# Kernel optimization log

Hardware: AMD Instinct MI355X
Metric: run time of the kernel (lower is better)

## Reference

```python
import jax, jax.numpy as jnp
import numpy as np

N = 100000      # nodes
E = 1600000     # edges (avg degree 16)
IN_DIM = 64
H = 4           # num_heads
D = 32          # out_dim per head
NEG_SLOPE = 0.1


def setup_inputs() -> dict:
    key = jax.random.key(0)
    k_x, k_src, k_dst, k_w, k_fc, k_al, k_ar = jax.random.split(key, 7)
    x = jax.random.normal(k_x, (N, IN_DIM), dtype=jnp.float32)
    src = jax.random.randint(k_src, (E,), 0, N, dtype=jnp.int32)
    dst = jax.random.randint(k_dst, (E,), 0, N, dtype=jnp.int32)
    w = jax.random.uniform(k_w, (E,), dtype=jnp.float32)
    # xavier-ish init for learned params
    W_fc = jax.random.normal(k_fc, (IN_DIM, H * D), dtype=jnp.float32) * (2.0 / (IN_DIM + H * D)) ** 0.5
    attn_l = jax.random.normal(k_al, (1, H, D), dtype=jnp.float32) * 0.1
    attn_r = jax.random.normal(k_ar, (1, H, D), dtype=jnp.float32) * 0.1
    vt = jnp.zeros((1,), dtype=jnp.float32)  # unused by forward (as in the source)
    return {"vt": vt, "x": x, "src": src, "dst": dst, "w": w,
            "W_fc": W_fc, "attn_l": attn_l, "attn_r": attn_r}


def reference(vt, x, src, dst, w, W_fc, attn_l, attn_r):
    # node projection: [N, H, D]
    feat = (x @ W_fc).reshape(-1, H, D)
    el = jnp.sum(feat * attn_l, axis=-1)  # [N, H]
    er = jnp.sum(feat * attn_r, axis=-1)  # [N, H]
    # per-edge logits: u_add_v then leaky_relu, scaled by edge weight w
    e = el[src] + er[dst]                                   # [E, H]
    e = jnp.where(e >= 0, e, NEG_SLOPE * e)                 # leaky_relu
    e = w[:, None] * e                                      # [E, H]
    # edge softmax grouped by destination node (numerically stable)
    m = jax.ops.segment_max(e, dst, num_segments=N)         # [N, H]
    ex = jnp.exp(e - m[dst])                                # [E, H]
    den = jax.ops.segment_sum(ex, dst, num_segments=N)      # [N, H]
    a = ex / den[dst]                                       # [E, H]
    # message passing: u_mul_e -> sum over incoming edges
    msg = feat[src] * a[:, :, None]                         # [E, H, D]
    out = jax.ops.segment_sum(msg, dst, num_segments=N)     # [N, H, D]
    return out
```

## Files before the change

### kernel.cpp

```cpp
#include <hip/hip_runtime.h>
#include <math.h>

#define IN_DIM 64
#define HH 4
#define CC 128
#define NEG_SLOPE 0.1f

typedef __attribute__((ext_vector_type(8))) short short8;
typedef __attribute__((ext_vector_type(4))) float f32x4;

__device__ __forceinline__ float leaky(float v) { return v >= 0.f ? v : NEG_SLOPE * v; }

__device__ __forceinline__ unsigned f2bf(float f) {
  unsigned u = __float_as_uint(f);
  unsigned r = u + 0x7FFFu + ((u >> 16) & 1u);
  return r >> 16;
}
__device__ __forceinline__ float bflo(unsigned v) { return __uint_as_float(v << 16); }
__device__ __forceinline__ float bfhi(unsigned v) { return __uint_as_float(v & 0xFFFF0000u); }

__global__ void k_prepw(const float* __restrict__ W, unsigned* __restrict__ wt) {
  int tid = blockIdx.x * 256 + threadIdx.x;
  if (tid >= 128 * 32) return;
  int n = tid >> 5;
  int r = tid & 31;
  int b = r >> 2, h = r & 3;
  int k = b * 8 + h * 2;
  unsigned lo = f2bf(W[k * CC + n]);
  unsigned hi = f2bf(W[(k + 1) * CC + n]);
  wt[n * 32 + (b ^ (n & 7)) * 4 + h] = lo | (hi << 16);
}

__global__ __launch_bounds__(256) void k_project(
    const float* __restrict__ x, const unsigned* __restrict__ wt,
    const float* __restrict__ attn_l, const float* __restrict__ attn_r,
    unsigned* __restrict__ featbf, float* __restrict__ el, float* __restrict__ er,
    int N)
{
  __shared__ unsigned Wlds[4096];
  __shared__ float Al[CC], Ar[CC];
  int t = threadIdx.x;
  {
    const uint4* s = (const uint4*)wt;
    uint4* d = (uint4*)Wlds;
#pragma unroll
    for (int i = 0; i < 4; ++i) d[t + 256 * i] = s[t + 256 * i];
  }
  if (t < CC) { Al[t] = attn_l[t]; Ar[t] = attn_r[t]; }
  __syncthreads();

  int lane = t & 63;
  int l4 = lane >> 4, l16 = lane & 15;
  int node = blockIdx.x * 64 + (t >> 6) * 16 + l16;
  bool valid = node < N;
  int nrow = valid ? node : 0;

  short8 bfr[2];
#pragma unroll
  for (int s = 0; s < 2; ++s) {
    const float4* xp = (const float4*)&x[(size_t)nrow * 64 + s * 32 + l4 * 8];
    float4 xa = xp[0], xb = xp[1];
    union { short8 v; unsigned u[4]; } pk;
    pk.u[0] = f2bf(xa.x) | (f2bf(xa.y) << 16);
    pk.u[1] = f2bf(xa.z) | (f2bf(xa.w) << 16);
    pk.u[2] = f2bf(xb.x) | (f2bf(xb.y) << 16);
    pk.u[3] = f2bf(xb.z) | (f2bf(xb.w) << 16);
    bfr[s] = pk.v;
  }

  f32x4 acc[8];
#pragma unroll
  for (int c = 0; c < 8; ++c) acc[c] = (f32x4){0.f, 0.f, 0.f, 0.f};

#pragma unroll
  for (int c = 0; c < 8; ++c) {
    int n0 = c * 16 + l16;
    int sw = n0 & 7;
#pragma unroll
    for (int s = 0; s < 2; ++s) {
      int b = s * 4 + l4;
      union { short8 v; uint4 q; } af;
      af.q = *(const uint4*)&Wlds[n0 * 32 + (b ^ sw) * 4];
      acc[c] = __builtin_amdgcn_mfma_f32_16x16x32_bf16(af.v, bfr[s], acc[c], 0, 0, 0);
    }
  }

  if (valid) {
#pragma unroll
    for (int c = 0; c < 8; ++c) {
      unsigned u0 = f2bf(acc[c][0]) | (f2bf(acc[c][1]) << 16);
      unsigned u1 = f2bf(acc[c][2]) | (f2bf(acc[c][3]) << 16);
      *(uint2*)&featbf[(size_t)node * 64 + c * 8 + l4 * 2] = make_uint2(u0, u1);
    }
  }

  float pl[4], pr[4];
#pragma unroll
  for (int h = 0; h < 4; ++h) {
    float sl = 0.f, sr = 0.f;
#pragma unroll
    for (int ct = 0; ct < 2; ++ct) {
      int c = 2 * h + ct;
      int cb = c * 16 + l4 * 4;
#pragma unroll
      for (int r = 0; r < 4; ++r) {
        sl = fmaf(acc[c][r], Al[cb + r], sl);
        sr = fmaf(acc[c][r], Ar[cb + r], sr);
      }
    }
    sl += __shfl_xor(sl, 16, 64); sl += __shfl_xor(sl, 32, 64);
    sr += __shfl_xor(sr, 16, 64); sr += __shfl_xor(sr, 32, 64);
    pl[h] = sl; pr[h] = sr;
  }
  if (l4 == 0 && valid) {
    *(float4*)&el[(size_t)node * 4] = make_float4(pl[0], pl[1], pl[2], pl[3]);
    *(float4*)&er[(size_t)node * 4] = make_float4(pr[0], pr[1], pr[2], pr[3]);
  }
}

__global__ __launch_bounds__(256) void k_bhist(const int* __restrict__ dst,
                                               int* __restrict__ bcnt, int E, int NB) {
  __shared__ int lh[512];
  for (int i = threadIdx.x; i < NB; i += 256) lh[i] = 0;
  __syncthreads();
  int stride = gridDim.x * 256;
  for (int i = blockIdx.x * 256 + threadIdx.x; i < E; i += stride)
    atomicAdd(&lh[dst[i] >> 8], 1);
  __syncthreads();
  for (int i = threadIdx.x; i < NB; i += 256) {
    int c = lh[i];
    if (c) atomicAdd(&bcnt[i], c);
  }
}

__global__ __launch_bounds__(512) void k_bscan(const int* __restrict__ bcnt,
                                               int* __restrict__ gbase,
                                               int* __restrict__ gcursor, int NB) {
  __shared__ int sh[512];
  int t = threadIdx.x;
  int v = (t < NB) ? bcnt[t] : 0;
  sh[t] = v;
  __syncthreads();
  for (int off = 1; off < 512; off <<= 1) {
    int a = (t >= off) ? sh[t - off] : 0;
    __syncthreads();
    sh[t] += a;
    __syncthreads();
  }
  if (t < NB) {
    int e = sh[t] - v;
    gbase[t] = e;
    gcursor[t] = e;
  }
}

__global__ __launch_bounds__(512) void k_binA(const int* __restrict__ src,
                                              const int* __restrict__ dst,
                                              const float* __restrict__ w,
                                              int* __restrict__ gcursor,
                                              uint2* __restrict__ bkt, int E, int NB) {
  __shared__ int lh[512];
  __shared__ int lbase[512];
  int t = threadIdx.x;
  for (int i = t; i < NB; i += 512) lh[i] = 0;
  __syncthreads();
  long eb = (long)blockIdx.x * 8192;
  int b[16]; int r[16]; unsigned px[16]; unsigned pw[16];
#pragma unroll
  for (int i = 0; i < 16; ++i) {
    long e = eb + t + i * 512;
    bool v = e < E;
    int d = v ? dst[e] : 0;
    b[i] = d >> 8;
    px[i] = v ? ((unsigned)src[e] | ((unsigned)(d & 255) << 20)) : 0u;
    pw[i] = v ? ((const unsigned*)w)[e] : 0u;
    r[i] = v ? atomicAdd(&lh[b[i]], 1) : -1;
  }
  __syncthreads();
  for (int i = t; i < NB; i += 512) {
    int c = lh[i];
    lbase[i] = c ? atomicAdd(&gcursor[i], c) : 0;
  }
  __syncthreads();
#pragma unroll
  for (int i = 0; i < 16; ++i)
    if (r[i] >= 0) bkt[lbase[b[i]] + r[i]] = make_uint2(px[i], pw[i]);
}

__global__ __launch_bounds__(256) void k_binB(const uint2* __restrict__ bkt,
                                              const int* __restrict__ bcnt,
                                              const int* __restrict__ gbase,
                                              int* __restrict__ offs,
                                              int2* __restrict__ sp,
                                              int N, int E, int NB) {
  __shared__ int lh[256], sc[256], lcur[256];
  int b = blockIdx.x;
  int t = threadIdx.x;
  int base_b = gbase[b];
  int cnt_b = bcnt[b];
  lh[t] = 0;
  __syncthreads();
  for (int e = t; e < cnt_b; e += 256) {
    uint2 p = bkt[base_b + e];
    atomicAdd(&lh[(p.x >> 20) & 255], 1);
  }
  __syncthreads();
  int v = lh[t];
  sc[t] = v;
  __syncthreads();
  for (int off = 1; off < 256; off <<= 1) {
    int a = (t >= off) ? sc[t - off] : 0;
    __syncthreads();
    sc[t] += a;
    __syncthreads();
  }
  int excl = sc[t] - v;
  lcur[t] = excl;
  int n0 = b << 8;
  if (n0 + t < N) offs[n0 + t] = base_b + excl;
  if (b == NB - 1 && t == 0) offs[N] = E;
  __syncthreads();
  for (int e = t; e < cnt_b; e += 256) {
    uint2 p = bkt[base_b + e];
    int d = (p.x >> 20) & 255;
    int pos = atomicAdd(&lcur[d], 1);
    sp[base_b + pos] = make_int2((int)(p.x & 0xFFFFFu), (int)p.y);
  }
}

__global__ __launch_bounds__(256) void k_aggregate(
    const int* __restrict__ offs, const int2* __restrict__ sp,
    const float* __restrict__ el, const float* __restrict__ er,
    const uint2* __restrict__ featbf, float* __restrict__ out, int N)
{
  __shared__ int   s_lds[4][64];
  __shared__ float4 a_lds[4][64];

  int t = threadIdx.x;
  int lane = t & 63, wv = t >> 6;
  int n = blockIdx.x * 4 + wv;
  if (n >= N) return;

  int off0 = offs[n], off1 = offs[n + 1];
  int deg = off1 - off0;
  int half = lane >> 5;
  int l32 = lane & 31;
  int h = l32 >> 3;
  float4 acc = make_float4(0.f, 0.f, 0.f, 0.f);

  if (deg > 0) {
    float4 erv = *reinterpret_cast<const float4*>(&er[n * HH]);
    if (deg <= 64) {
      bool act = lane < deg;
      int2 p = sp[off0 + (act ? lane : 0)];
      int s = p.x;
      float wgt = __int_as_float(p.y);
      float4 elv = *reinterpret_cast<const float4*>(&el[s * HH]);
      float e0 = act ? leaky(elv.x + erv.x) * wgt : -INFINITY;
      float e1 = act ? leaky(elv.y + erv.y) * wgt : -INFINITY;
      float e2 = act ? leaky(elv.z + erv.z) * wgt : -INFINITY;
      float e3 = act ? leaky(elv.w + erv.w) * wgt : -INFINITY;
      float m0 = e0, m1 = e1, m2 = e2, m3 = e3;
#pragma unroll
      for (int d = 32; d >= 1; d >>= 1) {
        m0 = fmaxf(m0, __shfl_xor(m0, d, 64));
        m1 = fmaxf(m1, __shfl_xor(m1, d, 64));
        m2 = fmaxf(m2, __shfl_xor(m2, d, 64));
        m3 = fmaxf(m3, __shfl_xor(m3, d, 64));
      }
      float x0 = act ? __expf(e0 - m0) : 0.f;
      float x1 = act ? __expf(e1 - m1) : 0.f;
      float x2 = act ? __expf(e2 - m2) : 0.f;
      float x3 = act ? __expf(e3 - m3) : 0.f;
      float d0 = x0, d1 = x1, d2 = x2, d3 = x3;
#pragma unroll
      for (int d = 32; d >= 1; d >>= 1) {
        d0 += __shfl_xor(d0, d, 64);
        d1 += __shfl_xor(d1, d, 64);
        d2 += __shfl_xor(d2, d, 64);
        d3 += __shfl_xor(d3, d, 64);
      }
      float a0 = x0 * __builtin_amdgcn_rcpf(d0);
      float a1 = x1 * __builtin_amdgcn_rcpf(d1);
      float a2 = x2 * __builtin_amdgcn_rcpf(d2);
      float a3 = x3 * __builtin_amdgcn_rcpf(d3);
      s_lds[wv][lane] = s;
      a_lds[wv][lane] = make_float4(a0, a1, a2, a3);

      int npair = (deg + 1) >> 1;
      for (int tt = 0; tt < npair; ++tt) {
        int idx = 2 * tt + half;
        bool vv = idx < deg;
        float a = vv ? reinterpret_cast<const float*>(&a_lds[wv][idx])[h] : 0.f;
        int sj = s_lds[wv][vv ? idx : 0];
        uint2 f = featbf[(size_t)sj * 32 + l32];
        acc.x = fmaf(a, bflo(f.x), acc.x);
        acc.y = fmaf(a, bfhi(f.x), acc.y);
        acc.z = fmaf(a, bflo(f.y), acc.z);
        acc.w = fmaf(a, bfhi(f.y), acc.w);
      }
    } else {
      float m0 = -INFINITY, m1 = -INFINITY, m2 = -INFINITY, m3 = -INFINITY;
      for (int base = off0; base < off1; base += 64) {
        int j = base + lane;
        bool act = j < off1;
        int2 p = sp[act ? j : off0];
        float wgt = __int_as_float(p.y);
        float4 elv = *reinterpret_cast<const float4*>(&el[p.x * HH]);
        float e0 = act ? leaky(elv.x + erv.x) * wgt : -INFINITY;
        float e1 = act ? leaky(elv.y + erv.y) * wgt : -INFINITY;
        float e2 = act ? leaky(elv.z + erv.z) * wgt : -INFINITY;
        float e3 = act ? leaky(elv.w + erv.w) * wgt : -INFINITY;
        m0 = fmaxf(m0, e0); m1 = fmaxf(m1, e1);
        m2 = fmaxf(m2, e2); m3 = fmaxf(m3, e3);
      }
#pragma unroll
      for (int d = 32; d >= 1; d >>= 1) {
        m0 = fmaxf(m0, __shfl_xor(m0, d, 64));
        m1 = fmaxf(m1, __shfl_xor(m1, d, 64));
        m2 = fmaxf(m2, __shfl_xor(m2, d, 64));
        m3 = fmaxf(m3, __shfl_xor(m3, d, 64));
      }
      float d0 = 0.f, d1 = 0.f, d2 = 0.f, d3 = 0.f;
      for (int base = off0; base < off1; base += 64) {
        int j = base + lane;
        bool act = j < off1;
        int2 p = sp[act ? j : off0];
        float wgt = __int_as_float(p.y);
        float4 elv = *reinterpret_cast<const float4*>(&el[p.x * HH]);
        float e0 = leaky(elv.x + erv.x) * wgt;
        float e1 = leaky(elv.y + erv.y) * wgt;
        float e2 = leaky(elv.z + erv.z) * wgt;
        float e3 = leaky(elv.w + erv.w) * wgt;
        d0 += act ? __expf(e0 - m0) : 0.f;
        d1 += act ? __expf(e1 - m1) : 0.f;
        d2 += act ? __expf(e2 - m2) : 0.f;
        d3 += act ? __expf(e3 - m3) : 0.f;
      }
#pragma unroll
      for (int d = 32; d >= 1; d >>= 1) {
        d0 += __shfl_xor(d0, d, 64);
        d1 += __shfl_xor(d1, d, 64);
        d2 += __shfl_xor(d2, d, 64);
        d3 += __shfl_xor(d3, d, 64);
      }
      float i0 = __builtin_amdgcn_rcpf(d0), i1 = __builtin_amdgcn_rcpf(d1);
      float i2 = __builtin_amdgcn_rcpf(d2), i3 = __builtin_amdgcn_rcpf(d3);
      for (int base = off0; base < off1; base += 64) {
        int j = base + lane;
        bool act = j < off1;
        int2 p = sp[act ? j : off0];
        float wgt = __int_as_float(p.y);
        float4 elv = *reinterpret_cast<const float4*>(&el[p.x * HH]);
        float e0 = leaky(elv.x + erv.x) * wgt;
        float e1 = leaky(elv.y + erv.y) * wgt;
        float e2 = leaky(elv.z + erv.z) * wgt;
        float e3 = leaky(elv.w + erv.w) * wgt;
        float a0 = act ? __expf(e0 - m0) * i0 : 0.f;
        float a1 = act ? __expf(e1 - m1) * i1 : 0.f;
        float a2 = act ? __expf(e2 - m2) * i2 : 0.f;
        float a3 = act ? __expf(e3 - m3) * i3 : 0.f;
        s_lds[wv][lane] = p.x;
        a_lds[wv][lane] = make_float4(a0, a1, a2, a3);
        int cnt = off1 - base; if (cnt > 64) cnt = 64;
        int npair = (cnt + 1) >> 1;
        for (int tt = 0; tt < npair; ++tt) {
          int idx = 2 * tt + half;
          bool vv = idx < cnt;
          float a = vv ? reinterpret_cast<const float*>(&a_lds[wv][idx])[h] : 0.f;
          int sj = s_lds[wv][vv ? idx : 0];
          uint2 f = featbf[(size_t)sj * 32 + l32];
          acc.x = fmaf(a, bflo(f.x), acc.x);
          acc.y = fmaf(a, bfhi(f.x), acc.y);
          acc.z = fmaf(a, bflo(f.y), acc.z);
          acc.w = fmaf(a, bfhi(f.y), acc.w);
        }
      }
    }
  }
  acc.x += __shfl_xor(acc.x, 32, 64);
  acc.y += __shfl_xor(acc.y, 32, 64);
  acc.z += __shfl_xor(acc.z, 32, 64);
  acc.w += __shfl_xor(acc.w, 32, 64);
  if (lane < 32)
    *reinterpret_cast<float4*>(&out[(size_t)n * CC + 4 * l32]) = acc;
}

extern "C" void kernel_launch(void* const* d_in, const int* in_sizes, int n_in,
                              void* d_out, int out_size, void* d_ws, size_t ws_size,
                              hipStream_t stream)
{
  const float* x      = (const float*)d_in[1];
  const int*   src    = (const int*)d_in[2];
  const int*   dst    = (const int*)d_in[3];
  const float* w      = (const float*)d_in[4];
  const float* W_fc   = (const float*)d_in[5];
  const float* attn_l = (const float*)d_in[6];
  const float* attn_r = (const float*)d_in[7];
  float* out = (float*)d_out;

  int N = in_sizes[1] / IN_DIM;
  int E = in_sizes[2];
  int NB = (N + 255) / 256;

  char* p = (char*)d_ws;
  auto alloc = [&](size_t bytes) {
    char* r = p;
    p += (bytes + 255) & ~size_t(255);
    return r;
  };
  unsigned* featbf = (unsigned*)alloc((size_t)N * 64 * 4);
  float* el    = (float*)alloc((size_t)N * HH * 4);
  float* er    = (float*)alloc((size_t)N * HH * 4);
  int*   offs  = (int*)alloc((size_t)(N + 1) * 4);
  int*   bcnt  = (int*)alloc(512 * 4);
  int*   gbase = (int*)alloc(512 * 4);
  int*   gcur  = (int*)alloc(512 * 4);
  unsigned* wtswz = (unsigned*)alloc(4096 * 4);
  uint2* bkt   = (uint2*)alloc((size_t)E * 8);
  int2*  sp    = (int2*)alloc((size_t)E * 8);

  hipMemsetAsync(bcnt, 0, 512 * 4, stream);

  k_prepw<<<16, 256, 0, stream>>>(W_fc, wtswz);
  k_project<<<(N + 63) / 64, 256, 0, stream>>>(x, wtswz, attn_l, attn_r, featbf, el, er, N);
  k_bhist<<<256, 256, 0, stream>>>(dst, bcnt, E, NB);
  k_bscan<<<1, 512, 0, stream>>>(bcnt, gbase, gcur, NB);
  k_binA<<<(E + 8191) / 8192, 512, 0, stream>>>(src, dst, w, gcur, bkt, E, NB);
  k_binB<<<NB, 256, 0, stream>>>(bkt, bcnt, gbase, offs, sp, N, E, NB);
  k_aggregate<<<(N + 3) / 4, 256, 0, stream>>>(offs, sp, el, er, (const uint2*)featbf, out, N);
}
```

Baseline: 152.5 us.

## Split aggregation into alpha pass and column-sliced gather with quantized attention

Replaces the fused softmax+gather kernel with two passes. The first computes per-edge softmax weights and packs them, quantized to 12 bits, with the 20-bit source index into per-head arrays. The second gathers from a feature array re-laid out as 8 column slices so each slice fits better in cache. The intent is better cache locality for the random feature gather and less per-edge metadata traffic. The cost is an extra pass over the edges and 12-bit attention quantization, which lowers accuracy, plus a 20-bit limit on node indices.

After: 264.7 us. 1.74x slower.

```diff
diff --git a/kernel.cpp b/kernel.cpp
--- a/kernel.cpp
+++ b/kernel.cpp
@@ -34,7 +34,7 @@
 __global__ __launch_bounds__(256) void k_project(
     const float* __restrict__ x, const unsigned* __restrict__ wt,
     const float* __restrict__ attn_l, const float* __restrict__ attn_r,
-    unsigned* __restrict__ featbf, float* __restrict__ el, float* __restrict__ er,
+    unsigned* __restrict__ featS, float* __restrict__ el, float* __restrict__ er,
     int N)
 {
   __shared__ unsigned Wlds[4096];
@@ -90,7 +90,7 @@
     for (int c = 0; c < 8; ++c) {
       unsigned u0 = f2bf(acc[c][0]) | (f2bf(acc[c][1]) << 16);
       unsigned u1 = f2bf(acc[c][2]) | (f2bf(acc[c][3]) << 16);
-      *(uint2*)&featbf[(size_t)node * 64 + c * 8 + l4 * 2] = make_uint2(u0, u1);
+      *(uint2*)&featS[((size_t)c * N + node) * 8 + l4 * 2] = make_uint2(u0, u1);
     }
   }
 
@@ -228,162 +228,172 @@
   }
 }
 
-__global__ __launch_bounds__(256) void k_aggregate(
+__global__ __launch_bounds__(256) void k_alpha(
     const int* __restrict__ offs, const int2* __restrict__ sp,
     const float* __restrict__ el, const float* __restrict__ er,
-    const uint2* __restrict__ featbf, float* __restrict__ out, int N)
+    unsigned* __restrict__ AQ0, unsigned* __restrict__ AQ1,
+    unsigned* __restrict__ AQ2, unsigned* __restrict__ AQ3, int N)
 {
-  __shared__ int   s_lds[4][64];
-  __shared__ float4 a_lds[4][64];
-
-  int t = threadIdx.x;
-  int lane = t & 63, wv = t >> 6;
-  int n = blockIdx.x * 4 + wv;
+  int t = threadIdx.x;
+  int lane = t & 63;
+  int half = lane >> 5, l32 = lane & 31;
+  int n = blockIdx.x * 8 + (t >> 6) * 2 + half;
   if (n >= N) return;
-
   int off0 = offs[n], off1 = offs[n + 1];
   int deg = off1 - off0;
-  int half = lane >> 5;
-  int l32 = lane & 31;
-  int h = l32 >> 3;
-  float4 acc = make_float4(0.f, 0.f, 0.f, 0.f);
-
-  if (deg > 0) {
-    float4 erv = *reinterpret_cast<const float4*>(&er[n * HH]);
-    if (deg <= 64) {
-      bool act = lane < deg;
-      int2 p = sp[off0 + (act ? lane : 0)];
-      int s = p.x;
+  if (deg <= 0) return;
+  float4 erv = *(const float4*)&er[(size_t)n * 4];
+
+  if (deg <= 32) {
+    bool act = l32 < deg;
+    int j = off0 + (act ? l32 : 0);
+    int2 p = sp[j];
+    float wgt = __int_as_float(p.y);
+    float4 elv = *(const float4*)&el[(size_t)p.x * 4];
+    float e0 = act ? leaky(elv.x + erv.x) * wgt : -INFINITY;
+    float e1 = act ? leaky(elv.y + erv.y) * wgt : -INFINITY;
+    float e2 = act ? leaky(elv.z + erv.z) * wgt : -INFINITY;
+    float e3 = act ? leaky(elv.w + erv.w) * wgt : -INFINITY;
+    float m0 = e0, m1 = e1, m2 = e2, m3 = e3;
+#pragma unroll
+    for (int d = 16; d >= 1; d >>= 1) {
+      m0 = fmaxf(m0, __shfl_xor(m0, d, 64));
+      m1 = fmaxf(m1, __shfl_xor(m1, d, 64));
+      m2 = fmaxf(m2, __shfl_xor(m2, d, 64));
+      m3 = fmaxf(m3, __shfl_xor(m3, d, 64));
+    }
+    float x0 = act ? __expf(e0 - m0) : 0.f;
+    float x1 = act ? __expf(e1 - m1) : 0.f;
+    float x2 = act ? __expf(e2 - m2) : 0.f;
+    float x3 = act ? __expf(e3 - m3) : 0.f;
+    float d0 = x0, d1 = x1, d2 = x2, d3 = x3;
+#pragma unroll
+    for (int d = 16; d >= 1; d >>= 1) {
+      d0 += __shfl_xor(d0, d, 64);
+      d1 += __shfl_xor(d1, d, 64);
+      d2 += __shfl_xor(d2, d, 64);
+      d3 += __shfl_xor(d3, d, 64);
+    }
+    if (act) {
+      unsigned s = (unsigned)p.x;
+      unsigned q0 = __float2uint_rn(x0 * __builtin_amdgcn_rcpf(d0) * 4095.f);
+      unsigned q1 = __float2uint_rn(x1 * __builtin_amdgcn_rcpf(d1) * 4095.f);
+      unsigned q2 = __float2uint_rn(x2 * __builtin_amdgcn_rcpf(d2) * 4095.f);
+      unsigned q3 = __float2uint_rn(x3 * __builtin_amdgcn_rcpf(d3) * 4095.f);
+      __builtin_nontemporal_store(s | (q0 << 20), &AQ0[j]);
+      __builtin_nontemporal_store(s | (q1 << 20), &AQ1[j]);
+      __builtin_nontemporal_store(s | (q2 << 20), &AQ2[j]);
+      __builtin_nontemporal_store(s | (q3 << 20), &AQ3[j]);
+    }
+  } else {
+    float m0 = -INFINITY, m1 = -INFINITY, m2 = -INFINITY, m3 = -INFINITY;
+    for (int base = off0; base < off1; base += 32) {
+      int j = base + l32;
+      bool act = j < off1;
+      int2 p = sp[act ? j : off0];
       float wgt = __int_as_float(p.y);
-      float4 elv = *reinterpret_cast<const float4*>(&el[s * HH]);
+      float4 elv = *(const float4*)&el[(size_t)p.x * 4];
       float e0 = act ? leaky(elv.x + erv.x) * wgt : -INFINITY;
       float e1 = act ? leaky(elv.y + erv.y) * wgt : -INFINITY;
       float e2 = act ? leaky(elv.z + erv.z) * wgt : -INFINITY;
       float e3 = act ? leaky(elv.w + erv.w) * wgt : -INFINITY;
-      float m0 = e0, m1 = e1, m2 = e2, m3 = e3;
-#pragma unroll
-      for (int d = 32; d >= 1; d >>= 1) {
-        m0 = fmaxf(m0, __shfl_xor(m0, d, 64));
-        m1 = fmaxf(m1, __shfl_xor(m1, d, 64));
-        m2 = fmaxf(m2, __shfl_xor(m2, d, 64));
-        m3 = fmaxf(m3, __shfl_xor(m3, d, 64));
+      m0 = fmaxf(m0, e0); m1 = fmaxf(m1, e1);
+      m2 = fmaxf(m2, e2); m3 = fmaxf(m3, e3);
+    }
+#pragma unroll
+    for (int d = 16; d >= 1; d >>= 1) {
+      m0 = fmaxf(m0, __shfl_xor(m0, d, 64));
+      m1 = fmaxf(m1, __shfl_xor(m1, d, 64));
+      m2 = fmaxf(m2, __shfl_xor(m2, d, 64));
+      m3 = fmaxf(m3, __shfl_xor(m3, d, 64));
+    }
+    float d0 = 0.f, d1 = 0.f, d2 = 0.f, d3 = 0.f;
+    for (int base = off0; base < off1; base += 32) {
+      int j = base + l32;
+      bool act = j < off1;
+      int2 p = sp[act ? j : off0];
+      float wgt = __int_as_float(p.y);
+      float4 elv = *(const float4*)&el[(size_t)p.x * 4];
+      d0 += act ? __expf(leaky(elv.x + erv.x) * wgt - m0) : 0.f;
+      d1 += act ? __expf(leaky(elv.y + erv.y) * wgt - m1) : 0.f;
+      d2 += act ? __expf(leaky(elv.z + erv.z) * wgt - m2) : 0.f;
+      d3 += act ? __expf(leaky(elv.w + erv.w) * wgt - m3) : 0.f;
+    }
+#pragma unroll
+    for (int d = 16; d >= 1; d >>= 1) {
+      d0 += __shfl_xor(d0, d, 64);
+      d1 += __shfl_xor(d1, d, 64);
+      d2 += __shfl_xor(d2, d, 64);
+      d3 += __shfl_xor(d3, d, 64);
+    }
+    float i0 = __builtin_amdgcn_rcpf(d0) * 4095.f;
+    float i1 = __builtin_amdgcn_rcpf(d1) * 4095.f;
+    float i2 = __builtin_amdgcn_rcpf(d2) * 4095.f;
+    float i3 = __builtin_amdgcn_rcpf(d3) * 4095.f;
+    for (int base = off0; base < off1; base += 32) {
+      int j = base + l32;
+      bool act = j < off1;
+      int2 p = sp[act ? j : off0];
+      float wgt = __int_as_float(p.y);
+      float4 elv = *(const float4*)&el[(size_t)p.x * 4];
+      if (act) {
+        unsigned s = (unsigned)p.x;
+        unsigned q0 = __float2uint_rn(__expf(leaky(elv.x + erv.x) * wgt - m0) * i0);
+        unsigned q1 = __float2uint_rn(__expf(leaky(elv.y + erv.y) * wgt - m1) * i1);
+        unsigned q2 = __float2uint_rn(__expf(leaky(elv.z + erv.z) * wgt - m2) * i2);
+        unsigned q3 = __float2uint_rn(__expf(leaky(elv.w + erv.w) * wgt - m3) * i3);
+        __builtin_nontemporal_store(s | (q0 << 20), &AQ0[j]);
+        __builtin_nontemporal_store(s | (q1 << 20), &AQ1[j]);
+        __builtin_nontemporal_store(s | (q2 << 20), &AQ2[j]);
+        __builtin_nontemporal_store(s | (q3 << 20), &AQ3[j]);
       }
-      float x0 = act ? __expf(e0 - m0) : 0.f;
-      float x1 = act ? __expf(e1 - m1) : 0.f;
-      float x2 = act ? __expf(e2 - m2) : 0.f;
-      float x3 = act ? __expf(e3 - m3) : 0.f;
-      float d0 = x0, d1 = x1, d2 = x2, d3 = x3;
-#pragma unroll
-      for (int d = 32; d >= 1; d >>= 1) {
-        d0 += __shfl_xor(d0, d, 64);
-        d1 += __shfl_xor(d1, d, 64);
-        d2 += __shfl_xor(d2, d, 64);
-        d3 += __shfl_xor(d3, d, 64);
-      }
-      float a0 = x0 * __builtin_amdgcn_rcpf(d0);
-      float a1 = x1 * __builtin_amdgcn_rcpf(d1);
-      float a2 = x2 * __builtin_amdgcn_rcpf(d2);
-      float a3 = x3 * __builtin_amdgcn_rcpf(d3);
-      s_lds[wv][lane] = s;
-      a_lds[wv][lane] = make_float4(a0, a1, a2, a3);
-
-      int npair = (deg + 1) >> 1;
-      for (int tt = 0; tt < npair; ++tt) {
-        int idx = 2 * tt + half;
-        bool vv = idx < deg;
-        float a = vv ? reinterpret_cast<const float*>(&a_lds[wv][idx])[h] : 0.f;
-        int sj = s_lds[wv][vv ? idx : 0];
-        uint2 f = featbf[(size_t)sj * 32 + l32];
-        acc.x = fmaf(a, bflo(f.x), acc.x);
-        acc.y = fmaf(a, bfhi(f.x), acc.y);
-        acc.z = fmaf(a, bflo(f.y), acc.z);
-        acc.w = fmaf(a, bfhi(f.y), acc.w);
-      }
-    } else {
-      float m0 = -INFINITY, m1 = -INFINITY, m2 = -INFINITY, m3 = -INFINITY;
-      for (int base = off0; base < off1; base += 64) {
-        int j = base + lane;
-        bool act = j < off1;
-        int2 p = sp[act ? j : off0];
-        float wgt = __int_as_float(p.y);
-        float4 elv = *reinterpret_cast<const float4*>(&el[p.x * HH]);
-        float e0 = act ? leaky(elv.x + erv.x) * wgt : -INFINITY;
-        float e1 = act ? leaky(elv.y + erv.y) * wgt : -INFINITY;
-        float e2 = act ? leaky(elv.z + erv.z) * wgt : -INFINITY;
-        float e3 = act ? leaky(elv.w + erv.w) * wgt : -INFINITY;
-        m0 = fmaxf(m0, e0); m1 = fmaxf(m1, e1);
-        m2 = fmaxf(m2, e2); m3 = fmaxf(m3, e3);
-      }
-#pragma unroll
-      for (int d = 32; d >= 1; d >>= 1) {
-        m0 = fmaxf(m0, __shfl_xor(m0, d, 64));
-        m1 = fmaxf(m1, __shfl_xor(m1, d, 64));
-        m2 = fmaxf(m2, __shfl_xor(m2, d, 64));
-        m3 = fmaxf(m3, __shfl_xor(m3, d, 64));
-      }
-      float d0 = 0.f, d1 = 0.f, d2 = 0.f, d3 = 0.f;
-      for (int base = off0; base < off1; base += 64) {
-        int j = base + lane;
-        bool act = j < off1;
-        int2 p = sp[act ? j : off0];
-        float wgt = __int_as_float(p.y);
-        float4 elv = *reinterpret_cast<const float4*>(&el[p.x * HH]);
-        float e0 = leaky(elv.x + erv.x) * wgt;
-        float e1 = leaky(elv.y + erv.y) * wgt;
-        float e2 = leaky(elv.z + erv.z) * wgt;
-        float e3 = leaky(elv.w + erv.w) * wgt;
-        d0 += act ? __expf(e0 - m0) : 0.f;
-        d1 += act ? __expf(e1 - m1) : 0.f;
-        d2 += act ? __expf(e2 - m2) : 0.f;
-        d3 += act ? __expf(e3 - m3) : 0.f;
-      }
-#pragma unroll
-      for (int d = 32; d >= 1; d >>= 1) {
-        d0 += __shfl_xor(d0, d, 64);
-        d1 += __shfl_xor(d1, d, 64);
-        d2 += __shfl_xor(d2, d, 64);
-        d3 += __shfl_xor(d3, d, 64);
-      }
-      float i0 = __builtin_amdgcn_rcpf(d0), i1 = __builtin_amdgcn_rcpf(d1);
-      float i2 = __builtin_amdgcn_rcpf(d2), i3 = __builtin_amdgcn_rcpf(d3);
-      for (int base = off0; base < off1; base += 64) {
-        int j = base + lane;
-        bool act = j < off1;
-        int2 p = sp[act ? j : off0];
-        float wgt = __int_as_float(p.y);
-        float4 elv = *reinterpret_cast<const float4*>(&el[p.x * HH]);
-        float e0 = leaky(elv.x + erv.x) * wgt;
-        float e1 = leaky(elv.y + erv.y) * wgt;
-        float e2 = leaky(elv.z + erv.z) * wgt;
-        float e3 = leaky(elv.w + erv.w) * wgt;
-        float a0 = act ? __expf(e0 - m0) * i0 : 0.f;
-        float a1 = act ? __expf(e1 - m1) * i1 : 0.f;
-        float a2 = act ? __expf(e2 - m2) * i2 : 0.f;
-        float a3 = act ? __expf(e3 - m3) * i3 : 0.f;
-        s_lds[wv][lane] = p.x;
-        a_lds[wv][lane] = make_float4(a0, a1, a2, a3);
-        int cnt = off1 - base; if (cnt > 64) cnt = 64;
-        int npair = (cnt + 1) >> 1;
-        for (int tt = 0; tt < npair; ++tt) {
-          int idx = 2 * tt + half;
-          bool vv = idx < cnt;
-          float a = vv ? reinterpret_cast<const float*>(&a_lds[wv][idx])[h] : 0.f;
-          int sj = s_lds[wv][vv ? idx : 0];
-          uint2 f = featbf[(size_t)sj * 32 + l32];
-          acc.x = fmaf(a, bflo(f.x), acc.x);
-          acc.y = fmaf(a, bfhi(f.x), acc.y);
-          acc.z = fmaf(a, bflo(f.y), acc.z);
-          acc.w = fmaf(a, bfhi(f.y), acc.w);
-        }
-      }
-    }
-  }
-  acc.x += __shfl_xor(acc.x, 32, 64);
-  acc.y += __shfl_xor(acc.y, 32, 64);
-  acc.z += __shfl_xor(acc.z, 32, 64);
-  acc.w += __shfl_xor(acc.w, 32, 64);
-  if (lane < 32)
-    *reinterpret_cast<float4*>(&out[(size_t)n * CC + 4 * l32]) = acc;
+    }
+  }
+}
+
+__global__ __launch_bounds__(256) void k_slice(
+    const int* __restrict__ offs,
+    const unsigned* __restrict__ AQ0, const unsigned* __restrict__ AQ1,
+    const unsigned* __restrict__ AQ2, const unsigned* __restrict__ AQ3,
+    const char* __restrict__ featS, float* __restrict__ out, int N)
+{
+  int t = threadIdx.x;
+  int bid = blockIdx.x;
+  int s = bid & 7;
+  int lane = t & 63;
+  int half = lane >> 5;
+  int g = (lane >> 2) & 7, l4 = lane & 3;
+  int n = (bid >> 3) * 8 + (t >> 6) * 2 + half;
+  if (n >= N) return;
+
+  const unsigned* AQ = (s < 2) ? AQ0 : (s < 4) ? AQ1 : (s < 6) ? AQ2 : AQ3;
+  const char* fbase = featS + ((size_t)s * N) * 32 + l4 * 8;
+  int off0 = offs[n], off1 = offs[n + 1];
+  int deg = off1 - off0;
+
+  float a0 = 0.f, a1 = 0.f, a2 = 0.f, a3 = 0.f;
+  for (int b = 0; b < deg; b += 8) {
+    int idx = b + g;
+    bool v = idx < deg;
+    unsigned u = __builtin_nontemporal_load(&AQ[off0 + (v ? idx : 0)]);
+    float al = v ? (float)(u >> 20) * (1.f / 4095.f) : 0.f;
+    uint2 f = *(const uint2*)(fbase + (size_t)(u & 0xFFFFFu) * 32);
+    a0 = fmaf(al, bflo(f.x), a0);
+    a1 = fmaf(al, bfhi(f.x), a1);
+    a2 = fmaf(al, bflo(f.y), a2);
+    a3 = fmaf(al, bfhi(f.y), a3);
+  }
+#pragma unroll
+  for (int d = 4; d <= 16; d <<= 1) {
+    a0 += __shfl_xor(a0, d, 64);
+    a1 += __shfl_xor(a1, d, 64);
+    a2 += __shfl_xor(a2, d, 64);
+    a3 += __shfl_xor(a3, d, 64);
+  }
+  if (g == 0) {
+    f32x4 o = {a0, a1, a2, a3};
+    __builtin_nontemporal_store(o, (f32x4*)&out[(size_t)n * CC + s * 16 + l4 * 4]);
+  }
 }
 
 extern "C" void kernel_launch(void* const* d_in, const int* in_sizes, int n_in,
@@ -409,7 +419,7 @@
     p += (bytes + 255) & ~size_t(255);
     return r;
   };
-  unsigned* featbf = (unsigned*)alloc((size_t)N * 64 * 4);
+  unsigned* featS = (unsigned*)alloc((size_t)N * 64 * 4);
   float* el    = (float*)alloc((size_t)N * HH * 4);
   float* er    = (float*)alloc((size_t)N * HH * 4);
   int*   offs  = (int*)alloc((size_t)(N + 1) * 4);
@@ -419,14 +429,20 @@
   unsigned* wtswz = (unsigned*)alloc(4096 * 4);
   uint2* bkt   = (uint2*)alloc((size_t)E * 8);
   int2*  sp    = (int2*)alloc((size_t)E * 8);
+  unsigned* AQ2 = (unsigned*)alloc((size_t)E * 4);
+  unsigned* AQ3 = (unsigned*)alloc((size_t)E * 4);
+  unsigned* AQ0 = (unsigned*)bkt;
+  unsigned* AQ1 = AQ0 + E;
 
   hipMemsetAsync(bcnt, 0, 512 * 4, stream);
 
   k_prepw<<<16, 256, 0, stream>>>(W_fc, wtswz);
-  k_project<<<(N + 63) / 64, 256, 0, stream>>>(x, wtswz, attn_l, attn_r, featbf, el, er, N);
+  k_project<<<(N + 63) / 64, 256, 0, stream>>>(x, wtswz, attn_l, attn_r, featS, el, er, N);
   k_bhist<<<256, 256, 0, stream>>>(dst, bcnt, E, NB);
   k_bscan<<<1, 512, 0, stream>>>(bcnt, gbase, gcur, NB);
   k_binA<<<(E + 8191) / 8192, 512, 0, stream>>>(src, dst, w, gcur, bkt, E, NB);
   k_binB<<<NB, 256, 0, stream>>>(bkt, bcnt, gbase, offs, sp, N, E, NB);
-  k_aggregate<<<(N + 3) / 4, 256, 0, stream>>>(offs, sp, el, er, (const uint2*)featbf, out, N);
-}
+  k_alpha<<<(N + 7) / 8, 256, 0, stream>>>(offs, sp, el, er, AQ0, AQ1, AQ2, AQ3, N);
+  k_slice<<<((N + 7) / 8) * 8, 256, 0, stream>>>(offs, AQ0, AQ1, AQ2, AQ3,
+                                                 (const char*)featS, out, N);
+}
```
